# Optimization experiments

Measured on AMD Instinct MI355X. Metric: run time of the kernel, lower is better.

## Reference

```python
import jax, jax.numpy as jnp
import numpy as np

K_SIZE = 5  # local window size (odd, SAME padding, stride 1)


def _local_attn(x_main, x_ref, W_main, W_ref, k_size=K_SIZE):
    # 1x1 convs == per-pixel channel matmuls
    cm = jnp.einsum('bhwc,cd->bhwd', x_main, W_main)  # query  [B,H,W,C']
    cr = jnp.einsum('bhwc,cd->bhwd', x_ref, W_ref)    # keys   [B,H,W,C']
    pad = (k_size - 1) // 2
    B, H, W, C = cr.shape
    crp = jnp.pad(cr, ((0, 0), (pad, pad), (pad, pad), (0, 0)))
    # score for each of the k*k offsets: dot(query, shifted key) per pixel.
    # Avoids materializing the [B,H,W,k*k,C] patch tensor.
    scores = [
        jnp.einsum('bhwc,bhwc->bhw', cm, crp[:, i:i + H, j:j + W, :])
        for i in range(k_size) for j in range(k_size)
    ]
    # the layer concatenates the query itself as the last "key" (self score)
    scores.append(jnp.einsum('bhwc,bhwc->bhw', cm, cm))
    attn = jnp.stack(scores, axis=-1)  # [B,H,W,k*k+1]
    return jax.nn.softmax(attn, axis=-1)


def setup_inputs() -> dict:
    key = jax.random.key(0)
    k1, k2, k3, k4 = jax.random.split(key, 4)
    B, H, W, C = 4, 128, 128, 64
    Ci = 64  # intermediate_dim
    return {
        'x_main': jax.random.normal(k1, (B, H, W, C), jnp.float32),
        'x_ref': jax.random.normal(k2, (B, H, W, C), jnp.float32),
        'W_main': jax.random.normal(k3, (C, Ci), jnp.float32) * (2.0 / C) ** 0.5,
        'W_ref': jax.random.normal(k4, (C, Ci), jnp.float32) * (2.0 / C) ** 0.5,
    }


def reference(x_main, x_ref, W_main, W_ref):
    return _local_attn(x_main, x_ref, W_main, W_ref)
```

## Files before the change

kernel.cpp:

```cpp
#include <hip/hip_runtime.h>
#include <math.h>

#define HDIM 128
#define WDIM 128
#define CDIM 64
#define BDIM 4

#define TILE_W 16
#define TILE_H 8
#define HALO_W 20
#define HALO_H 12
#define NHALO (HALO_W * HALO_H)
#define PSTRIDE 68
#define WSTRIDE 65

typedef short bf16x8 __attribute__((ext_vector_type(8)));
typedef float f32x4  __attribute__((ext_vector_type(4)));

__device__ __forceinline__ void split_bf16(float f, short& hi, short& lo) {
    unsigned u = __float_as_uint(f);
    hi = (short)(u >> 16);
    float hf = __uint_as_float(u & 0xffff0000u);
    float l  = f - hf;
    lo = (short)(__float_as_uint(l) >> 16);
}

__global__ __launch_bounds__(256, 1)
void fused_mfma_local_attn(const float* __restrict__ xm,
                           const float* __restrict__ xr,
                           const float* __restrict__ Wm,
                           const float* __restrict__ Wr,
                           float* __restrict__ out) {
    __shared__ float lds[16320];
    float* Wsh = lds;
    float* cms = lds + 4352;
    float* crs = lds;

    const int t    = threadIdx.x;
    const int lane = t & 63;
    const int wv   = t >> 6;
    const int m    = lane & 15;
    const int quad = lane >> 4;
    const int tx0  = blockIdx.x * TILE_W;
    const int ty0  = blockIdx.y * TILE_H;
    const int b    = blockIdx.z;

    #pragma unroll
    for (int i = 0; i < 16; ++i) {
        int L = t + 256 * i;
        Wsh[(L >> 6) * WSTRIDE + (L & 63)] = Wm[L];
    }
    __syncthreads();

    bf16x8 Bhi[2][4], Blo[2][4];
    #pragma unroll
    for (int ks = 0; ks < 2; ++ks)
        #pragma unroll
        for (int nt = 0; nt < 4; ++nt)
            #pragma unroll
            for (int j = 0; j < 8; ++j) {
                float f = Wsh[(ks * 32 + quad * 8 + j) * WSTRIDE + nt * 16 + m];
                short hi, lo; split_bf16(f, hi, lo);
                Bhi[ks][nt][j] = hi; Blo[ks][nt][j] = lo;
            }

    #pragma unroll
    for (int s = 0; s < 2; ++s) {
        const int tile = 2 * wv + s;
        const float* ap = xm + (((size_t)b * HDIM + ty0 + tile) * WDIM
                                + tx0 + m) * CDIM + quad * 8;
        float4 p0 = *(const float4*)(ap);
        float4 p1 = *(const float4*)(ap + 4);
        float4 p2 = *(const float4*)(ap + 32);
        float4 p3 = *(const float4*)(ap + 36);

        bf16x8 Ahi[2], Alo[2];
        {
            float fv[16] = {p0.x,p0.y,p0.z,p0.w, p1.x,p1.y,p1.z,p1.w,
                            p2.x,p2.y,p2.z,p2.w, p3.x,p3.y,p3.z,p3.w};
            #pragma unroll
            for (int ks = 0; ks < 2; ++ks)
                #pragma unroll
                for (int j = 0; j < 8; ++j) {
                    short hi, lo; split_bf16(fv[8 * ks + j], hi, lo);
                    Ahi[ks][j] = hi; Alo[ks][j] = lo;
                }
        }
        f32x4 acc[4];
        #pragma unroll
        for (int nt = 0; nt < 4; ++nt)
            { acc[nt][0]=0.f; acc[nt][1]=0.f; acc[nt][2]=0.f; acc[nt][3]=0.f; }
        #pragma unroll
        for (int ks = 0; ks < 2; ++ks)
            #pragma unroll
            for (int nt = 0; nt < 4; ++nt) {
                acc[nt] = __builtin_amdgcn_mfma_f32_16x16x32_bf16(Ahi[ks], Bhi[ks][nt], acc[nt], 0,0,0);
                acc[nt] = __builtin_amdgcn_mfma_f32_16x16x32_bf16(Ahi[ks], Blo[ks][nt], acc[nt], 0,0,0);
                acc[nt] = __builtin_amdgcn_mfma_f32_16x16x32_bf16(Alo[ks], Bhi[ks][nt], acc[nt], 0,0,0);
            }
        #pragma unroll
        for (int nt = 0; nt < 4; ++nt)
            #pragma unroll
            for (int r = 0; r < 4; ++r)
                cms[(tile * 16 + quad * 4 + r) * PSTRIDE + nt * 16 + m] = acc[nt][r];
    }
    __syncthreads();

    #pragma unroll
    for (int i = 0; i < 16; ++i) {
        int L = t + 256 * i;
        Wsh[(L >> 6) * WSTRIDE + (L & 63)] = Wr[L];
    }
    __syncthreads();

    #pragma unroll
    for (int ks = 0; ks < 2; ++ks)
        #pragma unroll
        for (int nt = 0; nt < 4; ++nt)
            #pragma unroll
            for (int j = 0; j < 8; ++j) {
                float f = Wsh[(ks * 32 + quad * 8 + j) * WSTRIDE + nt * 16 + m];
                short hi, lo; split_bf16(f, hi, lo);
                Bhi[ks][nt][j] = hi; Blo[ks][nt][j] = lo;
            }

    const int pl = t >> 1;
    const int cg = t & 1;
    float4 qv[8];
    #pragma unroll
    for (int mq = 0; mq < 8; ++mq)
        qv[mq] = *(const float4*)&cms[pl * PSTRIDE + cg * 32 + 4 * mq];
    __syncthreads();

    #pragma unroll
    for (int s = 0; s < 4; ++s) {
        const int tj = wv + 4 * s;
        if (tj < 15) {
            const int hp = tj * 16 + m;
            const int hy = hp / HALO_W;
            const int hx = hp - hy * HALO_W;
            const int gy = ty0 + hy - 2, gx = tx0 + hx - 2;
            float4 p0 = make_float4(0,0,0,0), p1 = p0, p2 = p0, p3 = p0;
            if (gy >= 0 && gy < HDIM && gx >= 0 && gx < WDIM) {
                const float* ap = xr + (((size_t)b * HDIM + gy) * WDIM + gx) * CDIM
                                  + quad * 8;
                p0 = *(const float4*)(ap);
                p1 = *(const float4*)(ap + 4);
                p2 = *(const float4*)(ap + 32);
                p3 = *(const float4*)(ap + 36);
            }
            bf16x8 Ahi[2], Alo[2];
            {
                float fv[16] = {p0.x,p0.y,p0.z,p0.w, p1.x,p1.y,p1.z,p1.w,
                                p2.x,p2.y,p2.z,p2.w, p3.x,p3.y,p3.z,p3.w};
                #pragma unroll
                for (int ks = 0; ks < 2; ++ks)
                    #pragma unroll
                    for (int j = 0; j < 8; ++j) {
                        short hi, lo; split_bf16(fv[8 * ks + j], hi, lo);
                        Ahi[ks][j] = hi; Alo[ks][j] = lo;
                    }
            }
            f32x4 acc[4];
            #pragma unroll
            for (int nt = 0; nt < 4; ++nt)
                { acc[nt][0]=0.f; acc[nt][1]=0.f; acc[nt][2]=0.f; acc[nt][3]=0.f; }
            #pragma unroll
            for (int ks = 0; ks < 2; ++ks)
                #pragma unroll
                for (int nt = 0; nt < 4; ++nt) {
                    acc[nt] = __builtin_amdgcn_mfma_f32_16x16x32_bf16(Ahi[ks], Bhi[ks][nt], acc[nt], 0,0,0);
                    acc[nt] = __builtin_amdgcn_mfma_f32_16x16x32_bf16(Ahi[ks], Blo[ks][nt], acc[nt], 0,0,0);
                    acc[nt] = __builtin_amdgcn_mfma_f32_16x16x32_bf16(Alo[ks], Bhi[ks][nt], acc[nt], 0,0,0);
                }
            #pragma unroll
            for (int nt = 0; nt < 4; ++nt)
                #pragma unroll
                for (int r = 0; r < 4; ++r)
                    crs[(tj * 16 + quad * 4 + r) * PSTRIDE + nt * 16 + m] = acc[nt][r];
        }
    }
    __syncthreads();

    const int lx = pl & (TILE_W - 1);
    const int ly = pl >> 4;
    const size_t gpx = ((size_t)b * HDIM + ty0 + ly) * WDIM + tx0 + lx;

    float s[26];
    #pragma unroll
    for (int k = 0; k < 25; ++k) {
        const int i = k / 5, j = k % 5;
        const int p = (ly + i) * HALO_W + (lx + j);
        const float4* kp = (const float4*)&crs[p * PSTRIDE + cg * 32];
        float acc = 0.f;
        #pragma unroll
        for (int mq = 0; mq < 8; ++mq) {
            float4 v = kp[mq];
            acc = fmaf(qv[mq].x, v.x, acc);
            acc = fmaf(qv[mq].y, v.y, acc);
            acc = fmaf(qv[mq].z, v.z, acc);
            acc = fmaf(qv[mq].w, v.w, acc);
        }
        s[k] = acc;
    }
    {
        float acc = 0.f;
        #pragma unroll
        for (int mq = 0; mq < 8; ++mq) {
            float4 v = qv[mq];
            acc = fmaf(v.x, v.x, acc);
            acc = fmaf(v.y, v.y, acc);
            acc = fmaf(v.z, v.z, acc);
            acc = fmaf(v.w, v.w, acc);
        }
        s[25] = acc;
    }

    #pragma unroll
    for (int k = 0; k < 26; ++k) s[k] += __shfl_xor(s[k], 1);

    float mx = s[0];
    #pragma unroll
    for (int k = 1; k < 26; ++k) mx = fmaxf(mx, s[k]);
    float sum = 0.f;
    #pragma unroll
    for (int k = 0; k < 26; ++k) { s[k] = __expf(s[k] - mx); sum += s[k]; }
    const float inv = 1.f / sum;

    float* op = &out[gpx * 26 + cg * 13];
    if (cg == 0) {
        #pragma unroll
        for (int k = 0; k < 13; ++k) op[k] = s[k] * inv;
    } else {
        #pragma unroll
        for (int k = 0; k < 13; ++k) op[k] = s[13 + k] * inv;
    }
}

extern "C" void kernel_launch(void* const* d_in, const int* in_sizes, int n_in,
                              void* d_out, int out_size, void* d_ws, size_t ws_size,
                              hipStream_t stream) {
    const float* xm = (const float*)d_in[0];
    const float* xr = (const float*)d_in[1];
    const float* Wm = (const float*)d_in[2];
    const float* Wr = (const float*)d_in[3];
    float* outp = (float*)d_out;

    dim3 g(WDIM / TILE_W, HDIM / TILE_H, BDIM);
    fused_mfma_local_attn<<<g, 256, 0, stream>>>(xm, xr, Wm, Wr, outp);
}
```

Baseline: 89.87 us.

## Prefetch weights and activation tiles into registers up front, allow two blocks per CU

```diff
diff --git a/kernel.cpp b/kernel.cpp
--- a/kernel.cpp
+++ b/kernel.cpp
@@ -25,7 +25,21 @@
     lo = (short)(__float_as_uint(l) >> 16);
 }
 
-__global__ __launch_bounds__(256, 1)
+__device__ __forceinline__ void build_A(const float4 p0, const float4 p1,
+                                        const float4 p2, const float4 p3,
+                                        bf16x8 Ahi[2], bf16x8 Alo[2]) {
+    float fv[16] = {p0.x,p0.y,p0.z,p0.w, p1.x,p1.y,p1.z,p1.w,
+                    p2.x,p2.y,p2.z,p2.w, p3.x,p3.y,p3.z,p3.w};
+    #pragma unroll
+    for (int ks = 0; ks < 2; ++ks)
+        #pragma unroll
+        for (int j = 0; j < 8; ++j) {
+            short hi, lo; split_bf16(fv[8 * ks + j], hi, lo);
+            Ahi[ks][j] = hi; Alo[ks][j] = lo;
+        }
+}
+
+__global__ __launch_bounds__(256, 2)
 void fused_mfma_local_attn(const float* __restrict__ xm,
                            const float* __restrict__ xr,
                            const float* __restrict__ Wm,
@@ -45,10 +59,48 @@
     const int ty0  = blockIdx.y * TILE_H;
     const int b    = blockIdx.z;
 
+    float wmv[16], wrv[16];
+    #pragma unroll
+    for (int i = 0; i < 16; ++i) wmv[i] = Wm[t + 256 * i];
+    #pragma unroll
+    for (int i = 0; i < 16; ++i) wrv[i] = Wr[t + 256 * i];
+
+    float4 am[2][4];
+    #pragma unroll
+    for (int s = 0; s < 2; ++s) {
+        const int tile = 2 * wv + s;
+        const float* ap = xm + (((size_t)b * HDIM + ty0 + tile) * WDIM
+                                + tx0 + m) * CDIM + quad * 8;
+        am[s][0] = *(const float4*)(ap);
+        am[s][1] = *(const float4*)(ap + 4);
+        am[s][2] = *(const float4*)(ap + 32);
+        am[s][3] = *(const float4*)(ap + 36);
+    }
+
+    float4 ar[2][4];
+    #pragma unroll
+    for (int s = 0; s < 2; ++s) {
+        const int tj = wv + 4 * s;
+        const int hp = tj * 16 + m;
+        const int hy = hp / HALO_W;
+        const int hx = hp - hy * HALO_W;
+        const int gy = ty0 + hy - 2, gx = tx0 + hx - 2;
+        float4 z = make_float4(0.f, 0.f, 0.f, 0.f);
+        ar[s][0] = z; ar[s][1] = z; ar[s][2] = z; ar[s][3] = z;
+        if (gy >= 0 && gy < HDIM && gx >= 0 && gx < WDIM) {
+            const float* ap = xr + (((size_t)b * HDIM + gy) * WDIM + gx) * CDIM
+                              + quad * 8;
+            ar[s][0] = *(const float4*)(ap);
+            ar[s][1] = *(const float4*)(ap + 4);
+            ar[s][2] = *(const float4*)(ap + 32);
+            ar[s][3] = *(const float4*)(ap + 36);
+        }
+    }
+
     #pragma unroll
     for (int i = 0; i < 16; ++i) {
         int L = t + 256 * i;
-        Wsh[(L >> 6) * WSTRIDE + (L & 63)] = Wm[L];
+        Wsh[(L >> 6) * WSTRIDE + (L & 63)] = wmv[i];
     }
     __syncthreads();
 
@@ -67,25 +119,8 @@
     #pragma unroll
     for (int s = 0; s < 2; ++s) {
         const int tile = 2 * wv + s;
-        const float* ap = xm + (((size_t)b * HDIM + ty0 + tile) * WDIM
-                                + tx0 + m) * CDIM + quad * 8;
-        float4 p0 = *(const float4*)(ap);
-        float4 p1 = *(const float4*)(ap + 4);
-        float4 p2 = *(const float4*)(ap + 32);
-        float4 p3 = *(const float4*)(ap + 36);
-
         bf16x8 Ahi[2], Alo[2];
-        {
-            float fv[16] = {p0.x,p0.y,p0.z,p0.w, p1.x,p1.y,p1.z,p1.w,
-                            p2.x,p2.y,p2.z,p2.w, p3.x,p3.y,p3.z,p3.w};
-            #pragma unroll
-            for (int ks = 0; ks < 2; ++ks)
-                #pragma unroll
-                for (int j = 0; j < 8; ++j) {
-                    short hi, lo; split_bf16(fv[8 * ks + j], hi, lo);
-                    Ahi[ks][j] = hi; Alo[ks][j] = lo;
-                }
-        }
+        build_A(am[s][0], am[s][1], am[s][2], am[s][3], Ahi, Alo);
         f32x4 acc[4];
         #pragma unroll
         for (int nt = 0; nt < 4; ++nt)
@@ -109,7 +144,7 @@
     #pragma unroll
     for (int i = 0; i < 16; ++i) {
         int L = t + 256 * i;
-        Wsh[(L >> 6) * WSTRIDE + (L & 63)] = Wr[L];
+        Wsh[(L >> 6) * WSTRIDE + (L & 63)] = wrv[i];
     }
     __syncthreads();
 
@@ -132,35 +167,35 @@
         qv[mq] = *(const float4*)&cms[pl * PSTRIDE + cg * 32 + 4 * mq];
     __syncthreads();
 
-    #pragma unroll
-    for (int s = 0; s < 4; ++s) {
-        const int tj = wv + 4 * s;
+    float4 ar2[2][4];
+    #pragma unroll
+    for (int s = 0; s < 2; ++s) {
+        const int tj = wv + 4 * (s + 2);
+        float4 z = make_float4(0.f, 0.f, 0.f, 0.f);
+        ar2[s][0] = z; ar2[s][1] = z; ar2[s][2] = z; ar2[s][3] = z;
         if (tj < 15) {
             const int hp = tj * 16 + m;
             const int hy = hp / HALO_W;
             const int hx = hp - hy * HALO_W;
             const int gy = ty0 + hy - 2, gx = tx0 + hx - 2;
-            float4 p0 = make_float4(0,0,0,0), p1 = p0, p2 = p0, p3 = p0;
             if (gy >= 0 && gy < HDIM && gx >= 0 && gx < WDIM) {
                 const float* ap = xr + (((size_t)b * HDIM + gy) * WDIM + gx) * CDIM
                                   + quad * 8;
-                p0 = *(const float4*)(ap);
-                p1 = *(const float4*)(ap + 4);
-                p2 = *(const float4*)(ap + 32);
-                p3 = *(const float4*)(ap + 36);
-            }
+                ar2[s][0] = *(const float4*)(ap);
+                ar2[s][1] = *(const float4*)(ap + 4);
+                ar2[s][2] = *(const float4*)(ap + 32);
+                ar2[s][3] = *(const float4*)(ap + 36);
+            }
+        }
+    }
+
+    #pragma unroll
+    for (int s = 0; s < 4; ++s) {
+        const int tj = wv + 4 * s;
+        if (tj < 15) {
+            const float4* pa = (s < 2) ? ar[s] : ar2[s - 2];
             bf16x8 Ahi[2], Alo[2];
-            {
-                float fv[16] = {p0.x,p0.y,p0.z,p0.w, p1.x,p1.y,p1.z,p1.w,
-                                p2.x,p2.y,p2.z,p2.w, p3.x,p3.y,p3.z,p3.w};
-                #pragma unroll
-                for (int ks = 0; ks < 2; ++ks)
-                    #pragma unroll
-                    for (int j = 0; j < 8; ++j) {
-                        short hi, lo; split_bf16(fv[8 * ks + j], hi, lo);
-                        Ahi[ks][j] = hi; Alo[ks][j] = lo;
-                    }
-            }
+            build_A(pa[0], pa[1], pa[2], pa[3], Ahi, Alo);
             f32x4 acc[4];
             #pragma unroll
             for (int nt = 0; nt < 4; ++nt)
```

New measurement: 90.99 us. About the same (+1.2%).
